# Kernel optimization log

Hardware: AMD Instinct MI355X
Metric: run time of the kernel (lower is better)

## Reference

```python
import jax, jax.numpy as jnp
import numpy as np
import itertools

R_MAX = 0.4
POWER = 0
B, N_ATOMS, K_OPS = 16, 256, 16

# 27 periodic image shifts, same order as itertools.product([0,1,-1], repeat=3)
SHIFTS = jnp.asarray(list(itertools.product([0, 1, -1], repeat=3)), dtype=jnp.float32)  # [27,3]


def _pair_sq_sum(f, r):
    """sum over neighbor pairs (dist<=r) of elementwise (frac_dst-frac_src)**2.

    Equivalent to torch get_neighbors (cdist over 27 shifted copies, radius
    mask, gather) followed by (vec*vec).sum(dim=0), without materializing
    the variable-length edge list. f: [N,3] -> out: [3]."""
    n = f.shape[0]
    # shift-major replication: f_ex[s*n + i] = f[i] + SHIFTS[s], matching
    # torch.cat([frac]*27) + shifts.repeat_interleave(n)
    f_ex = (f[None, :, :] + SHIFTS[:, None, :]).reshape(27 * n, 3)
    d = f_ex[None, :, :] - f[:, None, :]          # [N, 27N, 3] = dst - src
    dist2 = jnp.sum(d * d, axis=-1)               # [N, 27N]
    mask = (jnp.sqrt(dist2) <= r).astype(f.dtype)
    return jnp.einsum('ij,ijc->c', mask, d * d)   # [3]


def setup_inputs() -> dict:
    key = jax.random.key(0)
    k1, k2 = jax.random.split(key)
    fracs = jax.random.uniform(k1, (B * N_ATOMS, 3), dtype=jnp.float32)
    natms = jnp.full((B,), N_ATOMS, dtype=jnp.int32)
    oprss = jax.random.normal(k2, (B * K_OPS, 3, 3), dtype=jnp.float32)
    noprs = jnp.full((B,), K_OPS, dtype=jnp.int32)
    return {"fracs": fracs, "natms": natms, "oprss": oprss, "noprs": noprs}


def reference(fracs, natms, oprss, noprs):
    b = natms.shape[0]
    n = fracs.shape[0] // b          # uniform atoms per structure (static)
    k = oprss.shape[0] // noprs.shape[0]  # uniform operators per structure
    fr = fracs.reshape(b, n, 3)
    ops = oprss.reshape(b, k, 3, 3)
    r = R_MAX / (n ** POWER)

    def per_struct(loss, xs):
        f, opset = xs                        # [N,3], [K,3,3]
        out0 = _pair_sq_sum(f, r)            # identical for every opr

        def per_op(opr):
            f1 = (f @ opr.T) % 1.0
            return jnp.linalg.norm(_pair_sq_sum(f1, r) - out0)

        diffs = jax.vmap(per_op)(opset)      # [K]
        return loss + diffs.sum() / (k * b), None

    loss, _ = jax.lax.scan(per_struct, jnp.float32(0.0), (fr, ops))
    return loss
```

## Files before the change

kernel.cpp:

```cpp
#include <hip/hip_runtime.h>
#include <math.h>


#define NATOMS 256
#define KOPS   16
#define NB     16

__device__ __forceinline__ float wrap01(float x) {
    float m = fmodf(x, 1.0f);
    if (m < 0.0f) m += 1.0f;
    return m;
}

__global__ __launch_bounds__(1024) void sgo_kernel(
    const float* __restrict__ fracs,
    const float* __restrict__ oprss,
    float* __restrict__ ws,
    float* __restrict__ out)
{
    const int blk = blockIdx.x;
    const int b   = blk >> 4;
    const int k   = blk & 15;
    const int tid = threadIdx.x;
    const int i   = tid & 127;
    const int c   = tid >> 7;

    const float* f = fracs + (size_t)b * NATOMS * 3;

    __shared__ float4 idE[192], idO[192], opE[192], opO[192];

    if (tid < 512) {
        const int atom = tid & 255;
        float fx = f[atom*3+0], fy = f[atom*3+1], fz = f[atom*3+2];
        if (tid >= 256) {
            const float* op = oprss + (size_t)(b * KOPS + k) * 9;
            float gx = wrap01(fx*op[0] + fy*op[1] + fz*op[2]);
            float gy = wrap01(fx*op[3] + fy*op[4] + fz*op[5]);
            float gz = wrap01(fx*op[6] + fy*op[7] + fz*op[8]);
            fx = gx; fy = gy; fz = gz;
        }
        float4 v4 = make_float4(fx, fy, fz, 0.0f);
        float4* arrE = (tid < 256) ? idE : opE;
        float4* arrO = (tid < 256) ? idO : opO;
        const int slot = atom >> 1;
        if (atom & 1) arrO[slot] = v4; else arrE[slot] = v4;
        if (atom < 128) {
            if (atom & 1) arrO[128 + slot] = v4; else arrE[128 + slot] = v4;
        }
    }
    __syncthreads();

    const float4 ia = idE[i], ib = idO[i];
    const float4 oa = opE[i], ob = opO[i];

    float i2x=0.f,i2y=0.f,i2z=0.f, i1x=0.f,i1y=0.f,i1z=0.f;
    float o2x=0.f,o2y=0.f,o2z=0.f, o1x=0.f,o1y=0.f,o1z=0.f;

#define EVAL_INTO(FJ, S, AX, AY, AZ, SGN) do {                                 \
        float dx = (FJ).x - (S).x, dy = (FJ).y - (S).y, dz = (FJ).z - (S).z;   \
        float vx = dx - rintf(dx), vy = dy - rintf(dy), vz = dz - rintf(dz);   \
        float px = vx*vx, py = vy*vy, pz = vz*vz;                              \
        float d2 = px + py + pz;                                               \
        float m  = (d2 <= 0.16f) ? (SGN) : 0.0f;                               \
        AX = fmaf(px, m, AX); AY = fmaf(py, m, AY); AZ = fmaf(pz, m, AZ);      \
    } while (0)

    const int eb = i + 1 + 8 * c;
    #pragma unroll
    for (int u = 0; u < 8; ++u) {
        {   const float4 fj = idE[eb + u];
            EVAL_INTO(fj, ia, i2x, i2y, i2z, 1.0f);
            EVAL_INTO(fj, ib, i2x, i2y, i2z, 1.0f);
        }
        {   const float4 fj = opE[eb + u];
            EVAL_INTO(fj, oa, o2x, o2y, o2z, 1.0f);
            EVAL_INTO(fj, ob, o2x, o2y, o2z, 1.0f);
        }
        {   const float4 fj = idO[eb + u];
            EVAL_INTO(fj, ia, i2x, i2y, i2z, 1.0f);
            EVAL_INTO(fj, ib, i2x, i2y, i2z, 1.0f);
        }
        {   const float4 fj = opO[eb + u];
            EVAL_INTO(fj, oa, o2x, o2y, o2z, 1.0f);
            EVAL_INTO(fj, ob, o2x, o2y, o2z, 1.0f);
        }
    }

    if (c == 7) {
        EVAL_INTO(ib, ia, i2x, i2y, i2z, 1.0f);
        EVAL_INTO(ob, oa, o2x, o2y, o2z, 1.0f);
        {   const float4 fj = idE[i + 64];
            EVAL_INTO(fj, ia, i1x, i1y, i1z, -1.0f);
            EVAL_INTO(fj, ib, i1x, i1y, i1z, -1.0f);
        }
        {   const float4 fj = opE[i + 64];
            EVAL_INTO(fj, oa, o1x, o1y, o1z, -1.0f);
            EVAL_INTO(fj, ob, o1x, o1y, o1z, -1.0f);
        }
        {   const float4 fj = idO[i + 64];
            EVAL_INTO(fj, ia, i1x, i1y, i1z, -1.0f);
            EVAL_INTO(fj, ib, i1x, i1y, i1z, -1.0f);
        }
        {   const float4 fj = opO[i + 64];
            EVAL_INTO(fj, oa, o1x, o1y, o1z, -1.0f);
            EVAL_INTO(fj, ob, o1x, o1y, o1z, -1.0f);
        }
    }
#undef EVAL_INTO

    float dxr = fmaf(2.0f, o2x, o1x) - fmaf(2.0f, i2x, i1x);
    float dyr = fmaf(2.0f, o2y, o1y) - fmaf(2.0f, i2y, i1y);
    float dzr = fmaf(2.0f, o2z, o1z) - fmaf(2.0f, i2z, i1z);

    for (int off = 32; off >= 1; off >>= 1) {
        dxr += __shfl_xor(dxr, off);
        dyr += __shfl_xor(dyr, off);
        dzr += __shfl_xor(dzr, off);
    }
    __shared__ float part[16][3];
    const int wave = tid >> 6;
    if ((tid & 63) == 0) { part[wave][0] = dxr; part[wave][1] = dyr; part[wave][2] = dzr; }
    __syncthreads();

    if (tid == 0) {
        float sx = 0.f, sy = 0.f, sz = 0.f;
        #pragma unroll
        for (int w = 0; w < 16; ++w) {
            sx += part[w][0]; sy += part[w][1]; sz += part[w][2];
        }
        float v = sqrtf(sx*sx + sy*sy + sz*sz) * (1.0f / 256.0f);

        float*        partial = ws + (size_t)b * 64;
        unsigned int* ctrb    = (unsigned int*)(ws + 1024 + b * 64);
        float*        gacc    = ws + 2048;
        unsigned int* gctr    = (unsigned int*)(ws + 2064);

        float old = atomicAdd(partial, v);
        asm volatile("" : : "v"(old) : "memory");
        unsigned int o = atomicDec(ctrb, 15u);
        if (o == 1u) {
            float s = atomicExch(partial, 0.0f);
            asm volatile("" : : "v"(s) : "memory");
            float g = atomicAdd(gacc, s);
            asm volatile("" : : "v"(g) : "memory");
            unsigned int o2 = atomicDec(gctr, 15u);
            if (o2 == 1u) {
                float total = atomicExch(gacc, 0.0f);
                out[0] = total;
            }
        }
    }
}

extern "C" void kernel_launch(void* const* d_in, const int* in_sizes, int n_in,
                              void* d_out, int out_size, void* d_ws, size_t ws_size,
                              hipStream_t stream) {
    const float* fracs = (const float*)d_in[0];
    const float* oprss = (const float*)d_in[2];
    float* out = (float*)d_out;
    float* ws  = (float*)d_ws;

    sgo_kernel<<<NB * KOPS, 1024, 0, stream>>>(fracs, oprss, ws, out);
}
```

Baseline: 17.27 us.

## Split identity pair sum across operator blocks and replace atomic reduction with finish kernel

The identity-structure pair sum used to be recomputed in full by all 16 operator blocks of a structure. It is now split into slices, one per operator block, so each block computes only its share, which halves the per-block work and lets blocks use 512 threads instead of 1024. Per-block partial vectors go to a workspace, and a second single-block kernel combines them, computes the norms and sums the loss. This removes the atomic counter chain but adds a second kernel launch.

```diff
diff --git a/kernel.cpp b/kernel.cpp
--- a/kernel.cpp
+++ b/kernel.cpp
@@ -2,9 +2,8 @@
 #include <math.h>
 
 
-#define NATOMS 256
-#define KOPS   16
-#define NB     16
+#define NB   16
+#define KOPS 16
 
 __device__ __forceinline__ float wrap01(float x) {
     float m = fmodf(x, 1.0f);
@@ -12,24 +11,23 @@
     return m;
 }
 
-__global__ __launch_bounds__(1024) void sgo_kernel(
+__global__ __launch_bounds__(512) void pair_kernel(
     const float* __restrict__ fracs,
     const float* __restrict__ oprss,
-    float* __restrict__ ws,
-    float* __restrict__ out)
+    float4* __restrict__ rows)
 {
     const int blk = blockIdx.x;
     const int b   = blk >> 4;
     const int k   = blk & 15;
     const int tid = threadIdx.x;
     const int i   = tid & 127;
-    const int c   = tid >> 7;
+    const int c   = (tid >> 7) & 3;
 
-    const float* f = fracs + (size_t)b * NATOMS * 3;
+    const float* f = fracs + (size_t)b * 256 * 3;
 
     __shared__ float4 idE[192], idO[192], opE[192], opO[192];
 
-    if (tid < 512) {
+    {
         const int atom = tid & 255;
         float fx = f[atom*3+0], fy = f[atom*3+1], fz = f[atom*3+2];
         if (tid >= 256) {
@@ -40,21 +38,19 @@
             fx = gx; fy = gy; fz = gz;
         }
         float4 v4 = make_float4(fx, fy, fz, 0.0f);
-        float4* arrE = (tid < 256) ? idE : opE;
-        float4* arrO = (tid < 256) ? idO : opO;
+        float4* arr = (tid < 256) ? ((atom & 1) ? idO : idE)
+                                  : ((atom & 1) ? opO : opE);
         const int slot = atom >> 1;
-        if (atom & 1) arrO[slot] = v4; else arrE[slot] = v4;
-        if (atom < 128) {
-            if (atom & 1) arrO[128 + slot] = v4; else arrE[128 + slot] = v4;
-        }
+        arr[slot] = v4;
+        if (atom < 128) arr[128 + slot] = v4;
     }
     __syncthreads();
 
     const float4 ia = idE[i], ib = idO[i];
     const float4 oa = opE[i], ob = opO[i];
 
+    float o2x=0.f,o2y=0.f,o2z=0.f, o1x=0.f,o1y=0.f,o1z=0.f;
     float i2x=0.f,i2y=0.f,i2z=0.f, i1x=0.f,i1y=0.f,i1z=0.f;
-    float o2x=0.f,o2y=0.f,o2z=0.f, o1x=0.f,o1y=0.f,o1z=0.f;
 
 #define EVAL_INTO(FJ, S, AX, AY, AZ, SGN) do {                                 \
         float dx = (FJ).x - (S).x, dy = (FJ).y - (S).y, dz = (FJ).z - (S).z;   \
@@ -65,91 +61,108 @@
         AX = fmaf(px, m, AX); AY = fmaf(py, m, AY); AZ = fmaf(pz, m, AZ);      \
     } while (0)
 
-    const int eb = i + 1 + 8 * c;
-    #pragma unroll
-    for (int u = 0; u < 8; ++u) {
-        {   const float4 fj = idE[eb + u];
+    {
+        const int eb = i + 16 * c + 1;
+        #pragma unroll
+        for (int u = 0; u < 16; ++u) {
+            {   const float4 fj = opE[eb + u];
+                EVAL_INTO(fj, oa, o2x, o2y, o2z, 1.0f);
+                EVAL_INTO(fj, ob, o2x, o2y, o2z, 1.0f);
+            }
+            {   const float4 fj = opO[eb + u];
+                EVAL_INTO(fj, oa, o2x, o2y, o2z, 1.0f);
+                EVAL_INTO(fj, ob, o2x, o2y, o2z, 1.0f);
+            }
+        }
+    }
+    {
+        const int ebi = i + 4 * k + 1 + c;
+        {   const float4 fj = idE[ebi];
             EVAL_INTO(fj, ia, i2x, i2y, i2z, 1.0f);
             EVAL_INTO(fj, ib, i2x, i2y, i2z, 1.0f);
         }
-        {   const float4 fj = opE[eb + u];
-            EVAL_INTO(fj, oa, o2x, o2y, o2z, 1.0f);
-            EVAL_INTO(fj, ob, o2x, o2y, o2z, 1.0f);
-        }
-        {   const float4 fj = idO[eb + u];
+        {   const float4 fj = idO[ebi];
             EVAL_INTO(fj, ia, i2x, i2y, i2z, 1.0f);
             EVAL_INTO(fj, ib, i2x, i2y, i2z, 1.0f);
         }
-        {   const float4 fj = opO[eb + u];
-            EVAL_INTO(fj, oa, o2x, o2y, o2z, 1.0f);
-            EVAL_INTO(fj, ob, o2x, o2y, o2z, 1.0f);
-        }
     }
-
-    if (c == 7) {
-        EVAL_INTO(ib, ia, i2x, i2y, i2z, 1.0f);
+    if (c == 0) {
         EVAL_INTO(ob, oa, o2x, o2y, o2z, 1.0f);
-        {   const float4 fj = idE[i + 64];
-            EVAL_INTO(fj, ia, i1x, i1y, i1z, -1.0f);
-            EVAL_INTO(fj, ib, i1x, i1y, i1z, -1.0f);
-        }
+        if (k == 0) EVAL_INTO(ib, ia, i2x, i2y, i2z, 1.0f);
+    }
+    if (c == 3) {
         {   const float4 fj = opE[i + 64];
             EVAL_INTO(fj, oa, o1x, o1y, o1z, -1.0f);
             EVAL_INTO(fj, ob, o1x, o1y, o1z, -1.0f);
-        }
-        {   const float4 fj = idO[i + 64];
-            EVAL_INTO(fj, ia, i1x, i1y, i1z, -1.0f);
-            EVAL_INTO(fj, ib, i1x, i1y, i1z, -1.0f);
         }
         {   const float4 fj = opO[i + 64];
             EVAL_INTO(fj, oa, o1x, o1y, o1z, -1.0f);
             EVAL_INTO(fj, ob, o1x, o1y, o1z, -1.0f);
         }
+        if (k == 15) {
+            {   const float4 fj = idE[i + 64];
+                EVAL_INTO(fj, ia, i1x, i1y, i1z, -1.0f);
+                EVAL_INTO(fj, ib, i1x, i1y, i1z, -1.0f);
+            }
+            {   const float4 fj = idO[i + 64];
+                EVAL_INTO(fj, ia, i1x, i1y, i1z, -1.0f);
+                EVAL_INTO(fj, ib, i1x, i1y, i1z, -1.0f);
+            }
+        }
     }
 #undef EVAL_INTO
 
-    float dxr = fmaf(2.0f, o2x, o1x) - fmaf(2.0f, i2x, i1x);
-    float dyr = fmaf(2.0f, o2y, o1y) - fmaf(2.0f, i2y, i1y);
-    float dzr = fmaf(2.0f, o2z, o1z) - fmaf(2.0f, i2z, i1z);
+    float sox = fmaf(2.0f, o2x, o1x);
+    float soy = fmaf(2.0f, o2y, o1y);
+    float soz = fmaf(2.0f, o2z, o1z);
+    float six = fmaf(2.0f, i2x, i1x);
+    float siy = fmaf(2.0f, i2y, i1y);
+    float siz = fmaf(2.0f, i2z, i1z);
 
     for (int off = 32; off >= 1; off >>= 1) {
-        dxr += __shfl_xor(dxr, off);
-        dyr += __shfl_xor(dyr, off);
-        dzr += __shfl_xor(dzr, off);
+        sox += __shfl_xor(sox, off);  soy += __shfl_xor(soy, off);
+        soz += __shfl_xor(soz, off);  six += __shfl_xor(six, off);
+        siy += __shfl_xor(siy, off);  siz += __shfl_xor(siz, off);
     }
-    __shared__ float part[16][3];
+    __shared__ float part[8][6];
     const int wave = tid >> 6;
-    if ((tid & 63) == 0) { part[wave][0] = dxr; part[wave][1] = dyr; part[wave][2] = dzr; }
+    if ((tid & 63) == 0) {
+        part[wave][0] = sox; part[wave][1] = soy; part[wave][2] = soz;
+        part[wave][3] = six; part[wave][4] = siy; part[wave][5] = siz;
+    }
     __syncthreads();
+    if (tid == 0) {
+        float r0=0.f,r1=0.f,r2=0.f,r3=0.f,r4=0.f,r5=0.f;
+        #pragma unroll
+        for (int w = 0; w < 8; ++w) {
+            r0 += part[w][0]; r1 += part[w][1]; r2 += part[w][2];
+            r3 += part[w][3]; r4 += part[w][4]; r5 += part[w][5];
+        }
+        rows[blk]       = make_float4(r0, r1, r2, 0.0f);
+        rows[256 + blk] = make_float4(r3, r4, r5, 0.0f);
+    }
+}
 
-    if (tid == 0) {
-        float sx = 0.f, sy = 0.f, sz = 0.f;
-        #pragma unroll
-        for (int w = 0; w < 16; ++w) {
-            sx += part[w][0]; sy += part[w][1]; sz += part[w][2];
-        }
-        float v = sqrtf(sx*sx + sy*sy + sz*sz) * (1.0f / 256.0f);
+__global__ __launch_bounds__(256) void finish_kernel(
+    const float4* __restrict__ rows, float* __restrict__ out)
+{
+    const int t = threadIdx.x;
+    const int b = t >> 4;
+    const float4 so = rows[t];
+    float six = 0.f, siy = 0.f, siz = 0.f;
+    #pragma unroll
+    for (int k2 = 0; k2 < 16; ++k2) {
+        const float4 r = rows[256 + b * 16 + k2];
+        six += r.x; siy += r.y; siz += r.z;
+    }
+    float d0 = so.x - six, d1 = so.y - siy, d2 = so.z - siz;
+    float v = sqrtf(d0*d0 + d1*d1 + d2*d2);
 
-        float*        partial = ws + (size_t)b * 64;
-        unsigned int* ctrb    = (unsigned int*)(ws + 1024 + b * 64);
-        float*        gacc    = ws + 2048;
-        unsigned int* gctr    = (unsigned int*)(ws + 2064);
-
-        float old = atomicAdd(partial, v);
-        asm volatile("" : : "v"(old) : "memory");
-        unsigned int o = atomicDec(ctrb, 15u);
-        if (o == 1u) {
-            float s = atomicExch(partial, 0.0f);
-            asm volatile("" : : "v"(s) : "memory");
-            float g = atomicAdd(gacc, s);
-            asm volatile("" : : "v"(g) : "memory");
-            unsigned int o2 = atomicDec(gctr, 15u);
-            if (o2 == 1u) {
-                float total = atomicExch(gacc, 0.0f);
-                out[0] = total;
-            }
-        }
-    }
+    for (int off = 32; off >= 1; off >>= 1) v += __shfl_xor(v, off);
+    __shared__ float part[4];
+    if ((t & 63) == 0) part[t >> 6] = v;
+    __syncthreads();
+    if (t == 0) out[0] = (part[0] + part[1] + part[2] + part[3]) * (1.0f / 256.0f);
 }
 
 extern "C" void kernel_launch(void* const* d_in, const int* in_sizes, int n_in,
@@ -157,8 +170,9 @@
                               hipStream_t stream) {
     const float* fracs = (const float*)d_in[0];
     const float* oprss = (const float*)d_in[2];
-    float* out = (float*)d_out;
-    float* ws  = (float*)d_ws;
+    float* out   = (float*)d_out;
+    float4* rows = (float4*)d_ws;
 
-    sgo_kernel<<<NB * KOPS, 1024, 0, stream>>>(fracs, oprss, ws, out);
+    pair_kernel<<<NB * KOPS, 512, 0, stream>>>(fracs, oprss, rows);
+    finish_kernel<<<1, 256, 0, stream>>>(rows, out);
 }
```

New measurement: 14.46 us. 1.19x faster.
